# Kernel tuning notes

Hardware: AMD Instinct MI355X
Metric: run time of the kernel (lower is better)

## Reference

```python
import jax, jax.numpy as jnp
import numpy as np

MAX_ITER = 10
TAU = 1.0


def setup_inputs() -> dict:
    key = jax.random.key(0)
    k1, k2, k3 = jax.random.split(key, 3)
    B, R, C = 64, 1024, 1024
    s = jax.random.normal(k1, (B, R, C), dtype=jnp.float32)
    # nrows <= ncols per batch => no transposed_batch branch in the original
    nrows = jax.random.randint(k2, (B,), 128, 512).astype(jnp.int32)
    ncols = jax.random.randint(k3, (B,), 512, C + 1).astype(jnp.int32)
    return {"s": s, "nrows": nrows, "ncols": ncols}


def _masked_lse(x, mask, axis):
    """logsumexp over `axis` restricted to mask==True; finite-safe everywhere.
    Equivalent to torch.logsumexp after writing -inf into masked-out entries,
    but keeps all values finite so grads are clean."""
    neg = jnp.asarray(-1e30, x.dtype)
    m = jax.lax.stop_gradient(jnp.max(jnp.where(mask, x, neg), axis=axis, keepdims=True))
    e = jnp.where(mask, jnp.exp(jnp.where(mask, x, m) - m), jnp.zeros((), x.dtype))
    sum_e = jnp.sum(e, axis=axis, keepdims=True)
    any_m = jnp.any(mask, axis=axis, keepdims=True)
    return m + jnp.log(jnp.where(any_m, sum_e, jnp.ones((), x.dtype)))


def _sinkhorn(s, nrows, ncols):
    B, R, C = s.shape
    row_mask = (jnp.arange(R)[None, :] < nrows[:, None])[:, :, None]  # [B,R,1]
    col_mask = (jnp.arange(C)[None, :] < ncols[:, None])[:, None, :]  # [B,1,C]
    valid = row_mask & col_mask                                        # [B,R,C]
    log_s = s / TAU
    # Alternating row/col normalization in log space. In the original, entries
    # outside [nrows,ncols] are set to -inf and ignored by logsumexp; here we
    # keep them finite and mask inside the logsumexp, which is the same math
    # on the valid region, and we zero the invalid region at the end (exp(-inf)=0).
    for i in range(MAX_ITER):
        if i % 2 == 0:  # row normalization
            lse = _masked_lse(log_s, valid, axis=2)          # [B,R,1]
            log_s = log_s - jnp.where(row_mask, lse, 0.0)
        else:           # col normalization
            lse = _masked_lse(log_s, valid, axis=1)          # [B,1,C]
            log_s = log_s - jnp.where(col_mask, lse, 0.0)
    return jnp.where(valid, jnp.exp(log_s), jnp.zeros((), s.dtype))


def reference(s, nrows, ncols):
    return _sinkhorn(s, nrows, ncols)
```

## Files before the change

kernel.cpp:

```cpp
#include <hip/hip_runtime.h>
#include <hip/hip_fp16.h>


#define B_DIM 64
#define RCH 32
#define NCH 16

__device__ __forceinline__ float fast_rcp(float x) {
#if __has_builtin(__builtin_amdgcn_rcpf)
    return __builtin_amdgcn_rcpf(x);
#else
    return 1.0f / x;
#endif
}

__device__ __forceinline__ float wave_sum(float x) {
    #pragma unroll
    for (int off = 1; off < 64; off <<= 1) x += __shfl_xor(x, off);
    return x;
}

__device__ __forceinline__ float2 unpack2f(unsigned int u) {
    return __half22float2(__builtin_bit_cast(__half2, u));
}

__device__ __forceinline__ float dot16(
    const float4 A, const float4 B, const float4 w0, const float4 w1,
    const float4 w2, const float4 w3)
{
    float2 f; float s0, s1;
    f = unpack2f(__builtin_bit_cast(unsigned int, A.x)); s0 = f.x * w0.x;          s1 = f.y * w0.y;
    f = unpack2f(__builtin_bit_cast(unsigned int, A.y)); s0 = fmaf(f.x, w0.z, s0); s1 = fmaf(f.y, w0.w, s1);
    f = unpack2f(__builtin_bit_cast(unsigned int, A.z)); s0 = fmaf(f.x, w1.x, s0); s1 = fmaf(f.y, w1.y, s1);
    f = unpack2f(__builtin_bit_cast(unsigned int, A.w)); s0 = fmaf(f.x, w1.z, s0); s1 = fmaf(f.y, w1.w, s1);
    f = unpack2f(__builtin_bit_cast(unsigned int, B.x)); s0 = fmaf(f.x, w2.x, s0); s1 = fmaf(f.y, w2.y, s1);
    f = unpack2f(__builtin_bit_cast(unsigned int, B.y)); s0 = fmaf(f.x, w2.z, s0); s1 = fmaf(f.y, w2.w, s1);
    f = unpack2f(__builtin_bit_cast(unsigned int, B.z)); s0 = fmaf(f.x, w3.x, s0); s1 = fmaf(f.y, w3.y, s1);
    f = unpack2f(__builtin_bit_cast(unsigned int, B.w)); s0 = fmaf(f.x, w3.z, s0); s1 = fmaf(f.y, w3.w, s1);
    return s0 + s1;
}

__device__ __forceinline__ void phase2_col(
    const __half* __restrict__ E, const float* __restrict__ a_lds,
    float* __restrict__ cls,
    int b, int r0, int nr, int nc, int t, float* __restrict__ cs_cur)
{
    const int c0 = (t & 127) << 3;
    const int rsub = t >> 7;
    float acc0 = 0.f, acc1 = 0.f, acc2 = 0.f, acc3 = 0.f;
    float acc4 = 0.f, acc5 = 0.f, acc6 = 0.f, acc7 = 0.f;
    if (c0 < nc) {
        const int rs = r0 + (rsub << 3);
        const __half* __restrict__ Eb = E + ((size_t)b << 19) + c0;
        #pragma unroll
        for (int k = 0; k < 8; ++k) {
            const int r = rs + k;
            const float4 p = *reinterpret_cast<const float4*>(Eb + ((size_t)r << 10));
            const float av = a_lds[r - r0];
            const float2 f0 = unpack2f(__builtin_bit_cast(unsigned int, p.x));
            const float2 f1 = unpack2f(__builtin_bit_cast(unsigned int, p.y));
            const float2 f2 = unpack2f(__builtin_bit_cast(unsigned int, p.z));
            const float2 f3 = unpack2f(__builtin_bit_cast(unsigned int, p.w));
            acc0 = fmaf(f0.x, av, acc0); acc1 = fmaf(f0.y, av, acc1);
            acc2 = fmaf(f1.x, av, acc2); acc3 = fmaf(f1.y, av, acc3);
            acc4 = fmaf(f2.x, av, acc4); acc5 = fmaf(f2.y, av, acc5);
            acc6 = fmaf(f3.x, av, acc6); acc7 = fmaf(f3.y, av, acc7);
        }
    }
    float* dst = cls + (rsub << 10) + c0;
    *reinterpret_cast<float4*>(dst)     = make_float4(acc0, acc1, acc2, acc3);
    *reinterpret_cast<float4*>(dst + 4) = make_float4(acc4, acc5, acc6, acc7);
    __syncthreads();
    #pragma unroll
    for (int k = 0; k < 2; ++k) {
        const int c = t + (k << 9);
        const float v = cls[c] + cls[1024 + c] + cls[2048 + c] + cls[3072 + c];
        if (v != 0.f) atomicAdd(cs_cur + (b << 10) + c, v);
    }
}

__global__ __launch_bounds__(512) void pair_first(
    const float* __restrict__ s, const int* __restrict__ nrows,
    const int* __restrict__ ncols, __half* __restrict__ E,
    float* __restrict__ a, float* __restrict__ cs_cur,
    float* __restrict__ cs_next)
{
    const int b = blockIdx.y;
    const int rc = blockIdx.x;
    const int t = threadIdx.x;
    if (t < 64) cs_next[(b << 10) + (rc << 6) + t] = 0.f;

    const int nr = nrows[b];
    const int r0 = rc << 5;
    if (r0 >= nr) return;
    const int nc = ncols[b];

    __shared__ float a_lds[RCH];
    __shared__ float cls[4 * 1024];

    const int wave = t >> 6;
    const int lane = t & 63;
    const int cbase = lane << 4;
    const bool cOK = cbase < nc;

    #pragma unroll 1
    for (int k = 0; k < 4; ++k) {
        const int r = r0 + (wave << 2) + k;
        float sum = 0.f;
        if (r < nr && cOK) {
            const float* __restrict__ srow =
                s + ((size_t)b << 20) + ((size_t)r << 10) + cbase;
            __half* __restrict__ erow =
                E + ((size_t)b << 19) + ((size_t)r << 10) + cbase;
            float e[16];
            #pragma unroll
            for (int q = 0; q < 4; ++q) {
                const float4 x = *reinterpret_cast<const float4*>(srow + (q << 2));
                e[4 * q + 0] = __expf(x.x); e[4 * q + 1] = __expf(x.y);
                e[4 * q + 2] = __expf(x.z); e[4 * q + 3] = __expf(x.w);
            }
            #pragma unroll
            for (int j = 0; j < 16; ++j)
                if (cbase + j >= nc) e[j] = 0.f;
            __half2 h[8];
            #pragma unroll
            for (int q = 0; q < 8; ++q)
                h[q] = __floats2half2_rn(e[2 * q], e[2 * q + 1]);
            *reinterpret_cast<float4*>(erow)     = *reinterpret_cast<const float4*>(&h[0]);
            *reinterpret_cast<float4*>(erow + 8) = *reinterpret_cast<const float4*>(&h[4]);
            #pragma unroll
            for (int j = 0; j < 16; ++j) sum += e[j];
        }
        sum = wave_sum(sum);
        if (lane == 0) a_lds[(wave << 2) + k] = (r < nr) ? 1.0f / sum : 0.f;
    }
    __syncthreads();
    if (t < RCH) a[(b << 9) + r0 + t] = a_lds[t];

    phase2_col(E, a_lds, cls, b, r0, nr, nc, t, cs_cur);
}

__global__ __launch_bounds__(512) void pair_mid(
    const __half* __restrict__ E, const int* __restrict__ nrows,
    const int* __restrict__ ncols, const float* __restrict__ cs_prev,
    float* __restrict__ a, float* __restrict__ cs_cur,
    float* __restrict__ cs_next)
{
    const int b = blockIdx.y;
    const int rc = blockIdx.x;
    const int t = threadIdx.x;
    if (t < 64) cs_next[(b << 10) + (rc << 6) + t] = 0.f;

    const int nr = nrows[b];
    const int r0 = rc << 5;
    if (r0 >= nr) return;
    const int nc = ncols[b];

    __shared__ float a_lds[RCH];
    __shared__ float cls[4 * 1024];

    const int wave = t >> 6;
    const int lane = t & 63;
    const int cbase = lane << 4;

    float4 w0, w1, w2, w3;
    {
        const float* __restrict__ csp = cs_prev + (b << 10) + cbase;
        const float4 v0 = *reinterpret_cast<const float4*>(csp);
        const float4 v1 = *reinterpret_cast<const float4*>(csp + 4);
        const float4 v2 = *reinterpret_cast<const float4*>(csp + 8);
        const float4 v3 = *reinterpret_cast<const float4*>(csp + 12);
        w0.x = (cbase +  0 < nc) ? fast_rcp(v0.x) : 0.f;
        w0.y = (cbase +  1 < nc) ? fast_rcp(v0.y) : 0.f;
        w0.z = (cbase +  2 < nc) ? fast_rcp(v0.z) : 0.f;
        w0.w = (cbase +  3 < nc) ? fast_rcp(v0.w) : 0.f;
        w1.x = (cbase +  4 < nc) ? fast_rcp(v1.x) : 0.f;
        w1.y = (cbase +  5 < nc) ? fast_rcp(v1.y) : 0.f;
        w1.z = (cbase +  6 < nc) ? fast_rcp(v1.z) : 0.f;
        w1.w = (cbase +  7 < nc) ? fast_rcp(v1.w) : 0.f;
        w2.x = (cbase +  8 < nc) ? fast_rcp(v2.x) : 0.f;
        w2.y = (cbase +  9 < nc) ? fast_rcp(v2.y) : 0.f;
        w2.z = (cbase + 10 < nc) ? fast_rcp(v2.z) : 0.f;
        w2.w = (cbase + 11 < nc) ? fast_rcp(v2.w) : 0.f;
        w3.x = (cbase + 12 < nc) ? fast_rcp(v3.x) : 0.f;
        w3.y = (cbase + 13 < nc) ? fast_rcp(v3.y) : 0.f;
        w3.z = (cbase + 14 < nc) ? fast_rcp(v3.z) : 0.f;
        w3.w = (cbase + 15 < nc) ? fast_rcp(v3.w) : 0.f;
    }

    {
        const int rA = r0 + (wave << 2);
        const __half* __restrict__ Eb = E + ((size_t)b << 19) + cbase;
        const __half* __restrict__ e0 = Eb + ((size_t)(rA + 0) << 10);
        const __half* __restrict__ e1 = Eb + ((size_t)(rA + 1) << 10);
        const __half* __restrict__ e2 = Eb + ((size_t)(rA + 2) << 10);
        const __half* __restrict__ e3 = Eb + ((size_t)(rA + 3) << 10);
        const float4 A0 = *reinterpret_cast<const float4*>(e0);
        const float4 B0 = *reinterpret_cast<const float4*>(e0 + 8);
        const float4 A1 = *reinterpret_cast<const float4*>(e1);
        const float4 B1 = *reinterpret_cast<const float4*>(e1 + 8);
        const float4 A2 = *reinterpret_cast<const float4*>(e2);
        const float4 B2 = *reinterpret_cast<const float4*>(e2 + 8);
        const float4 A3 = *reinterpret_cast<const float4*>(e3);
        const float4 B3 = *reinterpret_cast<const float4*>(e3 + 8);

        float d0 = dot16(A0, B0, w0, w1, w2, w3);
        float d1 = dot16(A1, B1, w0, w1, w2, w3);
        float d2 = dot16(A2, B2, w0, w1, w2, w3);
        float d3 = dot16(A3, B3, w0, w1, w2, w3);
        d0 = wave_sum(d0);
        d1 = wave_sum(d1);
        d2 = wave_sum(d2);
        d3 = wave_sum(d3);
        if (lane == 0) {
            const int rr = wave << 2;
            a_lds[rr + 0] = (rA + 0 < nr) ? fast_rcp(d0) : 0.f;
            a_lds[rr + 1] = (rA + 1 < nr) ? fast_rcp(d1) : 0.f;
            a_lds[rr + 2] = (rA + 2 < nr) ? fast_rcp(d2) : 0.f;
            a_lds[rr + 3] = (rA + 3 < nr) ? fast_rcp(d3) : 0.f;
        }
    }
    __syncthreads();
    if (t < RCH) a[(b << 9) + r0 + t] = a_lds[t];

    phase2_col(E, a_lds, cls, b, r0, nr, nc, t, cs_cur);
}

__global__ __launch_bounds__(256) void out_step_f(
    const __half* __restrict__ E, const int* __restrict__ nrows,
    const int* __restrict__ ncols, const float* __restrict__ a,
    const float* __restrict__ cs, float* __restrict__ out)
{
    const int g = (blockIdx.x << 8) + threadIdx.x;
    const int b = g >> 18;
    const int rem = g & 262143;
    const int r = rem >> 8;
    const int c0 = (rem & 255) << 2;
    const int nr = nrows[b];
    const int nc = ncols[b];
    float4 o = make_float4(0.f, 0.f, 0.f, 0.f);
    if (r < nr && c0 < nc) {
        const float ar = a[(b << 9) + r];
        const uint2 raw = *reinterpret_cast<const uint2*>(
            E + ((size_t)b << 19) + ((size_t)r << 10) + c0);
        const float2 f01 = unpack2f(raw.x);
        const float2 f23 = unpack2f(raw.y);
        const float4 c4 = *reinterpret_cast<const float4*>(cs + (b << 10) + c0);
        o.x = f01.x * ar * fast_rcp(c4.x);
        o.y = (c0 + 1 < nc) ? f01.y * ar * fast_rcp(c4.y) : 0.f;
        o.z = (c0 + 2 < nc) ? f23.x * ar * fast_rcp(c4.z) : 0.f;
        o.w = (c0 + 3 < nc) ? f23.y * ar * fast_rcp(c4.w) : 0.f;
    }
    reinterpret_cast<float4*>(out)[g] = o;
}


extern "C" void kernel_launch(void* const* d_in, const int* in_sizes, int n_in,
                              void* d_out, int out_size, void* d_ws, size_t ws_size,
                              hipStream_t stream) {
    const float* s = (const float*)d_in[0];
    const int* nrows = (const int*)d_in[1];
    const int* ncols = (const int*)d_in[2];
    float* out = (float*)d_out;

    const size_t E_BYTES = (size_t)B_DIM * 512 * 1024 * 2;
    const size_t CS_ELEMS = (size_t)B_DIM * 1024;
    __half* E = (__half*)d_ws;
    float* a = (float*)((char*)d_ws + E_BYTES);
    float* cs0 = a + (size_t)B_DIM * 512;
    float* cs1 = cs0 + CS_ELEMS;
    float* cs2 = cs1 + CS_ELEMS;

    hipMemsetAsync(cs0, 0, CS_ELEMS * sizeof(float), stream);

    const dim3 grid(NCH, B_DIM);
    pair_first<<<grid, 512, 0, stream>>>(s, nrows, ncols, E, a, cs0, cs1);
    pair_mid<<<grid, 512, 0, stream>>>(E, nrows, ncols, cs0, a, cs1, cs2);
    pair_mid<<<grid, 512, 0, stream>>>(E, nrows, ncols, cs1, a, cs2, cs0);
    pair_mid<<<grid, 512, 0, stream>>>(E, nrows, ncols, cs2, a, cs0, cs1);
    pair_mid<<<grid, 512, 0, stream>>>(E, nrows, ncols, cs0, a, cs1, cs2);
    out_step_f<<<65536, 256, 0, stream>>>(E, nrows, ncols, a, cs1, out);
}
```

Baseline: 161.9 us.

## Fuse all Sinkhorn phases into one persistent cooperative kernel with grid syncs

Replaces the memset plus six separate kernel launches with a single cooperative launch of 512 blocks. Each block handles a 64-row slice of one batch, and grid-wide syncs separate the row and column phases. Block indices are mapped so each XCD works on its own batches, and the row scalings stay in LDS, so the output pass no longer rereads them from global memory. The unused upper half of the output is zeroed inside the phases, and the old multi-kernel path is kept as a fallback if the cooperative launch fails. The risks are grid-sync overhead, the need for all blocks to fit on the device at once (512 threads with 16KB of LDS each), and load imbalance from inactive blocks.

Result: slower. 524.7 us (+224.0%).

```diff
diff --git a/kernel.cpp b/kernel.cpp
--- a/kernel.cpp
+++ b/kernel.cpp
@@ -1,10 +1,10 @@
 #include <hip/hip_runtime.h>
 #include <hip/hip_fp16.h>
-
+#include <hip/hip_cooperative_groups.h>
+
+namespace cg = cooperative_groups;
 
 #define B_DIM 64
-#define RCH 32
-#define NCH 16
 
 __device__ __forceinline__ float fast_rcp(float x) {
 #if __has_builtin(__builtin_amdgcn_rcpf)
@@ -40,10 +40,259 @@
     return s0 + s1;
 }
 
+
+__global__ __launch_bounds__(512, 4) void sinkhorn_pers(
+    const float* __restrict__ s, const int* __restrict__ nrows,
+    const int* __restrict__ ncols, __half* __restrict__ E,
+    float* __restrict__ csA, float* __restrict__ csB,
+    float* __restrict__ csC, float* __restrict__ out)
+{
+    cg::grid_group grid = cg::this_grid();
+    __shared__ float a_lds[64];
+    __shared__ float cls[4 * 1024];
+
+    const int bid = blockIdx.x;
+    const int xcd = bid & 7;
+    const int j = bid >> 3;
+    const int rc = j & 7;
+    const int b = (xcd << 3) | (j >> 3);
+    const int r0 = rc << 6;
+    const int t = threadIdx.x;
+    const int wave = t >> 6;
+    const int lane = t & 63;
+    const int cbase = lane << 4;
+    const int nr = nrows[b];
+    const int nc = ncols[b];
+    const bool active = (r0 < nr);
+    const bool cOK = cbase < nc;
+
+    __half* __restrict__ Eb = E + ((size_t)b << 19);
+
+
+#define ZERO_SLICE(CS) do { \
+        if (t < 128) (CS)[(b << 10) + (rc << 7) + t] = 0.f; } while (0)
+
+#define ZERO_UPPER(Q) do { \
+        float4* __restrict__ zb_ = reinterpret_cast<float4*>( \
+            out + ((size_t)b << 20) + ((size_t)(512 + r0 + ((Q) << 4)) << 10)); \
+        const float4 z_ = make_float4(0.f, 0.f, 0.f, 0.f); \
+        _Pragma("unroll") \
+        for (int i_ = 0; i_ < 8; ++i_) zb_[(i_ << 9) + t] = z_; } while (0)
+
+#define COL_PHASE(CS) do { \
+        const int c0_ = (t & 127) << 3; \
+        const int rsub_ = t >> 7; \
+        float a0_=0.f,a1_=0.f,a2_=0.f,a3_=0.f,a4_=0.f,a5_=0.f,a6_=0.f,a7_=0.f; \
+        if (c0_ < nc) { \
+            const __half* __restrict__ Ep_ = Eb + ((size_t)(r0 + (rsub_ << 4)) << 10) + c0_; \
+            _Pragma("unroll") \
+            for (int k_ = 0; k_ < 16; ++k_) { \
+                const float4 p_ = *reinterpret_cast<const float4*>(Ep_ + ((size_t)k_ << 10)); \
+                const float av_ = a_lds[(rsub_ << 4) + k_]; \
+                const float2 f0_ = unpack2f(__builtin_bit_cast(unsigned int, p_.x)); \
+                const float2 f1_ = unpack2f(__builtin_bit_cast(unsigned int, p_.y)); \
+                const float2 f2_ = unpack2f(__builtin_bit_cast(unsigned int, p_.z)); \
+                const float2 f3_ = unpack2f(__builtin_bit_cast(unsigned int, p_.w)); \
+                a0_ = fmaf(f0_.x, av_, a0_); a1_ = fmaf(f0_.y, av_, a1_); \
+                a2_ = fmaf(f1_.x, av_, a2_); a3_ = fmaf(f1_.y, av_, a3_); \
+                a4_ = fmaf(f2_.x, av_, a4_); a5_ = fmaf(f2_.y, av_, a5_); \
+                a6_ = fmaf(f3_.x, av_, a6_); a7_ = fmaf(f3_.y, av_, a7_); \
+            } \
+        } \
+        float* dst_ = cls + (rsub_ << 10) + c0_; \
+        *reinterpret_cast<float4*>(dst_)     = make_float4(a0_, a1_, a2_, a3_); \
+        *reinterpret_cast<float4*>(dst_ + 4) = make_float4(a4_, a5_, a6_, a7_); \
+        __syncthreads(); \
+        _Pragma("unroll") \
+        for (int k_ = 0; k_ < 2; ++k_) { \
+            const int c_ = t + (k_ << 9); \
+            const float v_ = cls[c_] + cls[1024 + c_] + cls[2048 + c_] + cls[3072 + c_]; \
+            if (v_ != 0.f) atomicAdd((CS) + (b << 10) + c_, v_); \
+        } \
+        __syncthreads(); } while (0)
+
+#define ROW_PHASE(CSP) do { \
+        float4 w0_, w1_, w2_, w3_; \
+        { \
+            const float* __restrict__ csp_ = (CSP) + (b << 10) + cbase; \
+            const float4 v0_ = *reinterpret_cast<const float4*>(csp_); \
+            const float4 v1_ = *reinterpret_cast<const float4*>(csp_ + 4); \
+            const float4 v2_ = *reinterpret_cast<const float4*>(csp_ + 8); \
+            const float4 v3_ = *reinterpret_cast<const float4*>(csp_ + 12); \
+            w0_.x = (cbase+ 0 < nc) ? fast_rcp(v0_.x) : 0.f; \
+            w0_.y = (cbase+ 1 < nc) ? fast_rcp(v0_.y) : 0.f; \
+            w0_.z = (cbase+ 2 < nc) ? fast_rcp(v0_.z) : 0.f; \
+            w0_.w = (cbase+ 3 < nc) ? fast_rcp(v0_.w) : 0.f; \
+            w1_.x = (cbase+ 4 < nc) ? fast_rcp(v1_.x) : 0.f; \
+            w1_.y = (cbase+ 5 < nc) ? fast_rcp(v1_.y) : 0.f; \
+            w1_.z = (cbase+ 6 < nc) ? fast_rcp(v1_.z) : 0.f; \
+            w1_.w = (cbase+ 7 < nc) ? fast_rcp(v1_.w) : 0.f; \
+            w2_.x = (cbase+ 8 < nc) ? fast_rcp(v2_.x) : 0.f; \
+            w2_.y = (cbase+ 9 < nc) ? fast_rcp(v2_.y) : 0.f; \
+            w2_.z = (cbase+10 < nc) ? fast_rcp(v2_.z) : 0.f; \
+            w2_.w = (cbase+11 < nc) ? fast_rcp(v2_.w) : 0.f; \
+            w3_.x = (cbase+12 < nc) ? fast_rcp(v3_.x) : 0.f; \
+            w3_.y = (cbase+13 < nc) ? fast_rcp(v3_.y) : 0.f; \
+            w3_.z = (cbase+14 < nc) ? fast_rcp(v3_.z) : 0.f; \
+            w3_.w = (cbase+15 < nc) ? fast_rcp(v3_.w) : 0.f; \
+        } \
+        _Pragma("unroll") \
+        for (int q_ = 0; q_ < 2; ++q_) { \
+            const int rA_ = r0 + (q_ << 5) + (wave << 2); \
+            const __half* __restrict__ eb_ = Eb + cbase; \
+            const __half* __restrict__ e0_ = eb_ + ((size_t)(rA_ + 0) << 10); \
+            const __half* __restrict__ e1_ = eb_ + ((size_t)(rA_ + 1) << 10); \
+            const __half* __restrict__ e2_ = eb_ + ((size_t)(rA_ + 2) << 10); \
+            const __half* __restrict__ e3_ = eb_ + ((size_t)(rA_ + 3) << 10); \
+            const float4 A0_ = *reinterpret_cast<const float4*>(e0_); \
+            const float4 B0_ = *reinterpret_cast<const float4*>(e0_ + 8); \
+            const float4 A1_ = *reinterpret_cast<const float4*>(e1_); \
+            const float4 B1_ = *reinterpret_cast<const float4*>(e1_ + 8); \
+            const float4 A2_ = *reinterpret_cast<const float4*>(e2_); \
+            const float4 B2_ = *reinterpret_cast<const float4*>(e2_ + 8); \
+            const float4 A3_ = *reinterpret_cast<const float4*>(e3_); \
+            const float4 B3_ = *reinterpret_cast<const float4*>(e3_ + 8); \
+            float d0_ = wave_sum(dot16(A0_, B0_, w0_, w1_, w2_, w3_)); \
+            float d1_ = wave_sum(dot16(A1_, B1_, w0_, w1_, w2_, w3_)); \
+            float d2_ = wave_sum(dot16(A2_, B2_, w0_, w1_, w2_, w3_)); \
+            float d3_ = wave_sum(dot16(A3_, B3_, w0_, w1_, w2_, w3_)); \
+            if (lane == 0) { \
+                const int rr_ = (q_ << 5) + (wave << 2); \
+                a_lds[rr_ + 0] = (rA_ + 0 < nr) ? fast_rcp(d0_) : 0.f; \
+                a_lds[rr_ + 1] = (rA_ + 1 < nr) ? fast_rcp(d1_) : 0.f; \
+                a_lds[rr_ + 2] = (rA_ + 2 < nr) ? fast_rcp(d2_) : 0.f; \
+                a_lds[rr_ + 3] = (rA_ + 3 < nr) ? fast_rcp(d3_) : 0.f; \
+            } \
+        } \
+        __syncthreads(); } while (0)
+
+    ZERO_SLICE(csA);
+    ZERO_SLICE(csB);
+
+    if (active) {
+        #pragma unroll 1
+        for (int q = 0; q < 2; ++q) {
+            #pragma unroll 1
+            for (int k = 0; k < 4; ++k) {
+                const int rr = (q << 5) + (wave << 2) + k;
+                const int r = r0 + rr;
+                float sum = 0.f;
+                if (r < nr && cOK) {
+                    const float* __restrict__ srow =
+                        s + ((size_t)b << 20) + ((size_t)r << 10) + cbase;
+                    __half* __restrict__ erow = Eb + ((size_t)r << 10) + cbase;
+                    float e0, e1, e2, e3, e4, e5, e6, e7;
+                    float e8, e9, e10, e11, e12, e13, e14, e15;
+                    const float4 x0 = *reinterpret_cast<const float4*>(srow);
+                    const float4 x1 = *reinterpret_cast<const float4*>(srow + 4);
+                    const float4 x2 = *reinterpret_cast<const float4*>(srow + 8);
+                    const float4 x3 = *reinterpret_cast<const float4*>(srow + 12);
+                    e0 = __expf(x0.x); e1 = __expf(x0.y); e2 = __expf(x0.z); e3 = __expf(x0.w);
+                    e4 = __expf(x1.x); e5 = __expf(x1.y); e6 = __expf(x1.z); e7 = __expf(x1.w);
+                    e8 = __expf(x2.x); e9 = __expf(x2.y); e10 = __expf(x2.z); e11 = __expf(x2.w);
+                    e12 = __expf(x3.x); e13 = __expf(x3.y); e14 = __expf(x3.z); e15 = __expf(x3.w);
+                    if (cbase +  1 >= nc) e1 = 0.f;
+                    if (cbase +  2 >= nc) e2 = 0.f;
+                    if (cbase +  3 >= nc) e3 = 0.f;
+                    if (cbase +  4 >= nc) e4 = 0.f;
+                    if (cbase +  5 >= nc) e5 = 0.f;
+                    if (cbase +  6 >= nc) e6 = 0.f;
+                    if (cbase +  7 >= nc) e7 = 0.f;
+                    if (cbase +  8 >= nc) e8 = 0.f;
+                    if (cbase +  9 >= nc) e9 = 0.f;
+                    if (cbase + 10 >= nc) e10 = 0.f;
+                    if (cbase + 11 >= nc) e11 = 0.f;
+                    if (cbase + 12 >= nc) e12 = 0.f;
+                    if (cbase + 13 >= nc) e13 = 0.f;
+                    if (cbase + 14 >= nc) e14 = 0.f;
+                    if (cbase + 15 >= nc) e15 = 0.f;
+                    const __half2 h0 = __floats2half2_rn(e0, e1);
+                    const __half2 h1 = __floats2half2_rn(e2, e3);
+                    const __half2 h2 = __floats2half2_rn(e4, e5);
+                    const __half2 h3 = __floats2half2_rn(e6, e7);
+                    const __half2 h4 = __floats2half2_rn(e8, e9);
+                    const __half2 h5 = __floats2half2_rn(e10, e11);
+                    const __half2 h6 = __floats2half2_rn(e12, e13);
+                    const __half2 h7 = __floats2half2_rn(e14, e15);
+                    float4 pkA, pkB;
+                    pkA.x = __builtin_bit_cast(float, h0); pkA.y = __builtin_bit_cast(float, h1);
+                    pkA.z = __builtin_bit_cast(float, h2); pkA.w = __builtin_bit_cast(float, h3);
+                    pkB.x = __builtin_bit_cast(float, h4); pkB.y = __builtin_bit_cast(float, h5);
+                    pkB.z = __builtin_bit_cast(float, h6); pkB.w = __builtin_bit_cast(float, h7);
+                    *reinterpret_cast<float4*>(erow)     = pkA;
+                    *reinterpret_cast<float4*>(erow + 8) = pkB;
+                    sum = (((e0 + e1) + (e2 + e3)) + ((e4 + e5) + (e6 + e7)))
+                        + (((e8 + e9) + (e10 + e11)) + ((e12 + e13) + (e14 + e15)));
+                }
+                sum = wave_sum(sum);
+                if (lane == 0) a_lds[rr] = (r < nr) ? fast_rcp(sum) : 0.f;
+            }
+        }
+        __syncthreads();
+    }
+
+    grid.sync();
+    if (active) COL_PHASE(csA);
+    grid.sync();
+
+    ZERO_SLICE(csC);
+    ZERO_UPPER(0);
+    if (active) { ROW_PHASE(csA); COL_PHASE(csB); }
+    grid.sync();
+
+    ZERO_SLICE(csA);
+    ZERO_UPPER(1);
+    if (active) { ROW_PHASE(csB); COL_PHASE(csC); }
+    grid.sync();
+
+    ZERO_SLICE(csB);
+    ZERO_UPPER(2);
+    if (active) { ROW_PHASE(csC); COL_PHASE(csA); }
+    grid.sync();
+
+    ZERO_UPPER(3);
+    if (active) { ROW_PHASE(csA); COL_PHASE(csB); }
+    grid.sync();
+
+    {
+        const float* __restrict__ csb = csB + (b << 10);
+        float* __restrict__ ob = out + ((size_t)b << 20);
+        #pragma unroll 1
+        for (int i = 0; i < 32; ++i) {
+            const int idx = (i << 9) + t;
+            const int rr = idx >> 8;
+            const int c0 = (idx & 255) << 2;
+            const int r = r0 + rr;
+            float4 o = make_float4(0.f, 0.f, 0.f, 0.f);
+            if (r < nr && c0 < nc) {
+                const float ar = a_lds[rr];
+                const uint2 raw = *reinterpret_cast<const uint2*>(
+                    Eb + ((size_t)r << 10) + c0);
+                const float2 f01 = unpack2f(raw.x);
+                const float2 f23 = unpack2f(raw.y);
+                const float4 c4v = *reinterpret_cast<const float4*>(csb + c0);
+                o.x = f01.x * ar * fast_rcp(c4v.x);
+                o.y = (c0 + 1 < nc) ? f01.y * ar * fast_rcp(c4v.y) : 0.f;
+                o.z = (c0 + 2 < nc) ? f23.x * ar * fast_rcp(c4v.z) : 0.f;
+                o.w = (c0 + 3 < nc) ? f23.y * ar * fast_rcp(c4v.w) : 0.f;
+            }
+            *reinterpret_cast<float4*>(ob + ((size_t)r << 10) + c0) = o;
+        }
+    }
+#undef ZERO_SLICE
+#undef ZERO_UPPER
+#undef COL_PHASE
+#undef ROW_PHASE
+}
+
+
+#define RCH 32
+#define NCH 16
+
 __device__ __forceinline__ void phase2_col(
     const __half* __restrict__ E, const float* __restrict__ a_lds,
-    float* __restrict__ cls,
-    int b, int r0, int nr, int nc, int t, float* __restrict__ cs_cur)
+    float* __restrict__ cls, int b, int r0, int nr, int nc, int t,
+    float* __restrict__ cs_cur)
 {
     const int c0 = (t & 127) << 3;
     const int rsub = t >> 7;
@@ -120,8 +369,8 @@
                 e[4 * q + 2] = __expf(x.z); e[4 * q + 3] = __expf(x.w);
             }
             #pragma unroll
-            for (int j = 0; j < 16; ++j)
-                if (cbase + j >= nc) e[j] = 0.f;
+            for (int jj = 0; jj < 16; ++jj)
+                if (cbase + jj >= nc) e[jj] = 0.f;
             __half2 h[8];
             #pragma unroll
             for (int q = 0; q < 8; ++q)
@@ -129,7 +378,7 @@
             *reinterpret_cast<float4*>(erow)     = *reinterpret_cast<const float4*>(&h[0]);
             *reinterpret_cast<float4*>(erow + 8) = *reinterpret_cast<const float4*>(&h[4]);
             #pragma unroll
-            for (int j = 0; j < 16; ++j) sum += e[j];
+            for (int jj = 0; jj < 16; ++jj) sum += e[jj];
         }
         sum = wave_sum(sum);
         if (lane == 0) a_lds[(wave << 2) + k] = (r < nr) ? 1.0f / sum : 0.f;
@@ -204,14 +453,10 @@
         const float4 A3 = *reinterpret_cast<const float4*>(e3);
         const float4 B3 = *reinterpret_cast<const float4*>(e3 + 8);
 
-        float d0 = dot16(A0, B0, w0, w1, w2, w3);
-        float d1 = dot16(A1, B1, w0, w1, w2, w3);
-        float d2 = dot16(A2, B2, w0, w1, w2, w3);
-        float d3 = dot16(A3, B3, w0, w1, w2, w3);
-        d0 = wave_sum(d0);
-        d1 = wave_sum(d1);
-        d2 = wave_sum(d2);
-        d3 = wave_sum(d3);
+        float d0 = wave_sum(dot16(A0, B0, w0, w1, w2, w3));
+        float d1 = wave_sum(dot16(A1, B1, w0, w1, w2, w3));
+        float d2 = wave_sum(dot16(A2, B2, w0, w1, w2, w3));
+        float d3 = wave_sum(dot16(A3, B3, w0, w1, w2, w3));
         if (lane == 0) {
             const int rr = wave << 2;
             a_lds[rr + 0] = (rA + 0 < nr) ? fast_rcp(d0) : 0.f;
@@ -271,8 +516,17 @@
     float* cs1 = cs0 + CS_ELEMS;
     float* cs2 = cs1 + CS_ELEMS;
 
+    {
+        void* args[] = {(void*)&s, (void*)&nrows, (void*)&ncols, (void*)&E,
+                        (void*)&cs0, (void*)&cs1, (void*)&cs2, (void*)&out};
+        hipError_t err = hipLaunchCooperativeKernel(
+            reinterpret_cast<const void*>(sinkhorn_pers),
+            dim3(512), dim3(512), args, 0, stream);
+        if (err == hipSuccess) return;
+        (void)hipGetLastError();
+    }
+
     hipMemsetAsync(cs0, 0, CS_ELEMS * sizeof(float), stream);
-
     const dim3 grid(NCH, B_DIM);
     pair_first<<<grid, 512, 0, stream>>>(s, nrows, ncols, E, a, cs0, cs1);
     pair_mid<<<grid, 512, 0, stream>>>(E, nrows, ncols, cs0, a, cs1, cs2);
```

## Zero unused output rows inside pair_mid kernels and halve final output grid

Applied to the files above, without the earlier changes.

Rows 512-1023 of each batch's output are always zero, since nrows is below 512. They are now written as zeros by the four pair_mid kernels, each covering a quarter of those rows before its early-return check. The final out_step_f kernel then covers only the first 512 rows with half as many blocks. The aim is to spread the zero-fill stores across the compute-bound iterations instead of doing them in a separate pass, at the cost of extra store traffic in each pair_mid.

After: 172.2 us. 6.3% more time.

```diff
diff --git a/kernel.cpp b/kernel.cpp
--- a/kernel.cpp
+++ b/kernel.cpp
@@ -144,12 +144,21 @@
     const __half* __restrict__ E, const int* __restrict__ nrows,
     const int* __restrict__ ncols, const float* __restrict__ cs_prev,
     float* __restrict__ a, float* __restrict__ cs_cur,
-    float* __restrict__ cs_next)
+    float* __restrict__ cs_next, float* __restrict__ out, const int zphase)
 {
     const int b = blockIdx.y;
     const int rc = blockIdx.x;
     const int t = threadIdx.x;
     if (t < 64) cs_next[(b << 10) + (rc << 6) + t] = 0.f;
+
+    {
+        const int zr = 512 + ((zphase - 1) << 7) + (rc << 3);
+        float4* __restrict__ zb = reinterpret_cast<float4*>(
+            out + ((size_t)b << 20) + ((size_t)zr << 10));
+        const float4 z = make_float4(0.f, 0.f, 0.f, 0.f);
+        #pragma unroll
+        for (int i = 0; i < 4; ++i) zb[(i << 9) + t] = z;
+    }
 
     const int nr = nrows[b];
     const int r0 = rc << 5;
@@ -204,14 +213,10 @@
         const float4 A3 = *reinterpret_cast<const float4*>(e3);
         const float4 B3 = *reinterpret_cast<const float4*>(e3 + 8);
 
-        float d0 = dot16(A0, B0, w0, w1, w2, w3);
-        float d1 = dot16(A1, B1, w0, w1, w2, w3);
-        float d2 = dot16(A2, B2, w0, w1, w2, w3);
-        float d3 = dot16(A3, B3, w0, w1, w2, w3);
-        d0 = wave_sum(d0);
-        d1 = wave_sum(d1);
-        d2 = wave_sum(d2);
-        d3 = wave_sum(d3);
+        float d0 = wave_sum(dot16(A0, B0, w0, w1, w2, w3));
+        float d1 = wave_sum(dot16(A1, B1, w0, w1, w2, w3));
+        float d2 = wave_sum(dot16(A2, B2, w0, w1, w2, w3));
+        float d3 = wave_sum(dot16(A3, B3, w0, w1, w2, w3));
         if (lane == 0) {
             const int rr = wave << 2;
             a_lds[rr + 0] = (rA + 0 < nr) ? fast_rcp(d0) : 0.f;
@@ -232,8 +237,8 @@
     const float* __restrict__ cs, float* __restrict__ out)
 {
     const int g = (blockIdx.x << 8) + threadIdx.x;
-    const int b = g >> 18;
-    const int rem = g & 262143;
+    const int b = g >> 17;
+    const int rem = g & 131071;
     const int r = rem >> 8;
     const int c0 = (rem & 255) << 2;
     const int nr = nrows[b];
@@ -251,7 +256,8 @@
         o.z = (c0 + 2 < nc) ? f23.x * ar * fast_rcp(c4.z) : 0.f;
         o.w = (c0 + 3 < nc) ? f23.y * ar * fast_rcp(c4.w) : 0.f;
     }
-    reinterpret_cast<float4*>(out)[g] = o;
+    *reinterpret_cast<float4*>(
+        out + ((size_t)b << 20) + ((size_t)r << 10) + c0) = o;
 }
 
 
@@ -275,9 +281,9 @@
 
     const dim3 grid(NCH, B_DIM);
     pair_first<<<grid, 512, 0, stream>>>(s, nrows, ncols, E, a, cs0, cs1);
-    pair_mid<<<grid, 512, 0, stream>>>(E, nrows, ncols, cs0, a, cs1, cs2);
-    pair_mid<<<grid, 512, 0, stream>>>(E, nrows, ncols, cs1, a, cs2, cs0);
-    pair_mid<<<grid, 512, 0, stream>>>(E, nrows, ncols, cs2, a, cs0, cs1);
-    pair_mid<<<grid, 512, 0, stream>>>(E, nrows, ncols, cs0, a, cs1, cs2);
-    out_step_f<<<65536, 256, 0, stream>>>(E, nrows, ncols, a, cs1, out);
-}
+    pair_mid<<<grid, 512, 0, stream>>>(E, nrows, ncols, cs0, a, cs1, cs2, out, 1);
+    pair_mid<<<grid, 512, 0, stream>>>(E, nrows, ncols, cs1, a, cs2, cs0, out, 2);
+    pair_mid<<<grid, 512, 0, stream>>>(E, nrows, ncols, cs2, a, cs0, cs1, out, 3);
+    pair_mid<<<grid, 512, 0, stream>>>(E, nrows, ncols, cs0, a, cs1, cs2, out, 4);
+    out_step_f<<<32768, 256, 0, stream>>>(E, nrows, ncols, a, cs1, out);
+}
```
